# Performance work log

Measured on AMD Instinct MI355X. Metric: run time of the kernel, lower is better.

The kernel has to match this reference:

```python
import jax, jax.numpy as jnp
import numpy as np

B, N, H, W = 2, 1024, 128, 128
SH_K = 27  # (sh_degree+1)^2 * 3 for sh_degree=2
L_L1, L_SSIM, L_DEPTH, L_OPAC = 0.8, 0.2, 0.5, 0.01
C0 = 0.28209479177387814


def _quat_to_rot(q):
    # q: [..., 4] (w,x,y,z) -> [..., 3, 3]
    w, x, y, z = q[..., 0], q[..., 1], q[..., 2], q[..., 3]
    R = jnp.stack([1 - 2 * (y * y + z * z), 2 * (x * y - w * z), 2 * (x * z + w * y),
                   2 * (x * y + w * z), 1 - 2 * (x * x + z * z), 2 * (y * z - w * x),
                   2 * (x * z - w * y), 2 * (y * z + w * x), 1 - 2 * (x * x + y * y)], axis=-1)
    return R.reshape(q.shape[:-1] + (3, 3))


def _ssim_window(size=7, sigma=1.5):
    coords = np.arange(size, dtype=np.float32) - size // 2
    g = np.exp(-coords ** 2 / (2 * sigma ** 2))
    g = g / g.sum()
    w2 = np.outer(g, g).astype(np.float32)
    return jnp.asarray(np.broadcast_to(w2[None, None], (3, 1, size, size)))  # OIHW, groups=3


def _dwconv(img, w):
    return jax.lax.conv_general_dilated(img, w, (1, 1), 'SAME',
                                        dimension_numbers=('NCHW', 'OIHW', 'NCHW'),
                                        feature_group_count=3)


def _ssim(img1, img2):
    C1, C2 = 0.01 ** 2, 0.03 ** 2
    w = _ssim_window()
    mu1, mu2 = _dwconv(img1, w), _dwconv(img2, w)
    s1 = _dwconv(img1 * img1, w) - mu1 ** 2
    s2 = _dwconv(img2 * img2, w) - mu2 ** 2
    s12 = _dwconv(img1 * img2, w) - mu1 * mu2
    return jnp.mean((2 * mu1 * mu2 + C1) * (2 * s12 + C2) /
                    ((mu1 ** 2 + mu2 ** 2 + C1) * (s1 + s2 + C2)))


def _render(gaussians, intrinsics):
    means = gaussians[:, :, :3]
    scales = gaussians[:, :, 3:6]
    rots = gaussians[:, :, 6:10]
    opac = gaussians[:, :, 10]        # [B,N]
    sh = gaussians[:, :, 11:]
    fx = intrinsics[:, 0, 0][:, None]
    fy = intrinsics[:, 1, 1][:, None]
    cx = intrinsics[:, 0, 2][:, None]
    cy = intrinsics[:, 1, 2][:, None]
    z = jnp.maximum(means[:, :, 2], 1e-4)
    px = fx * means[:, :, 0] / z + cx
    py = fy * means[:, :, 1] / z + cy
    # ---- 2D covariance (EWA) ----
    R = _quat_to_rot(rots)                               # [B,N,3,3]
    RS = R * scales[:, :, None, :]                        # R @ diag(s)
    cov3d = RS @ jnp.swapaxes(RS, -1, -2)
    zc = jnp.maximum(means[:, :, 2], 1e-6)
    zsq = zc * zc
    J = jnp.zeros(means.shape[:2] + (2, 3), means.dtype)
    J = J.at[:, :, 0, 0].set(fx / zc)
    J = J.at[:, :, 0, 2].set(-fx * means[:, :, 0] / zsq)
    J = J.at[:, :, 1, 1].set(fy / zc)
    J = J.at[:, :, 1, 2].set(-fy * means[:, :, 1] / zsq)
    cov2d = J @ cov3d @ jnp.swapaxes(J, -1, -2) + 0.3 * jnp.eye(2, dtype=means.dtype)
    det = jnp.maximum(cov2d[:, :, 0, 0] * cov2d[:, :, 1, 1] -
                      cov2d[:, :, 0, 1] * cov2d[:, :, 1, 0], 1e-8)
    inv00 = cov2d[:, :, 1, 1] / det
    inv11 = cov2d[:, :, 0, 0] / det
    inv01 = -cov2d[:, :, 0, 1] / det
    colors = jnp.clip(sh[:, :, :3] * C0 + 0.5, 0.0, 1.0)  # [B,N,3]
    # ---- dense per-pixel splatting ----
    gy = jnp.arange(H, dtype=means.dtype)
    gx = jnp.arange(W, dtype=means.dtype)
    dx = gx[None, None, None, :] - px[:, :, None, None]   # [B,N,1,W] -> bcast [B,N,H,W]
    dy = gy[None, None, :, None] - py[:, :, None, None]
    power = -0.5 * (inv00[:, :, None, None] * dx * dx +
                    2.0 * inv01[:, :, None, None] * dx * dy +
                    inv11[:, :, None, None] * dy * dy)
    alpha = jnp.exp(jnp.clip(power, -10.0, 0.0)) * opac[:, :, None, None]
    alpha = jnp.minimum(alpha, 0.99)
    # ---- depth sort + front-to-back compositing ----
    order = jnp.argsort(z, axis=1)
    alpha_s = jnp.take_along_axis(alpha, order[:, :, None, None], axis=1)
    colors_s = jnp.take_along_axis(colors, order[:, :, None], axis=1)
    depth_s = jnp.take_along_axis(z, order, axis=1)
    cp = jnp.cumprod(1.0 - alpha_s, axis=1)
    Tr = jnp.concatenate([jnp.ones_like(alpha_s[:, :1]), cp[:, :-1]], axis=1)
    weights = Tr * alpha_s                               # [B,N,H,W]
    rgb = jnp.clip(jnp.einsum('bnhw,bnc->bchw', weights, colors_s), 0.0, 1.0)
    depth = jnp.sum(weights * depth_s[:, :, None, None], axis=1, keepdims=True)
    return rgb, depth


def setup_inputs() -> dict:
    key = jax.random.key(0)
    k = jax.random.split(key, 8)
    xy = jax.random.normal(k[0], (B, N, 2)) * 1.0
    zc = jax.random.uniform(k[1], (B, N, 1), minval=0.5, maxval=4.0)
    scales = jax.random.uniform(k[2], (B, N, 3), minval=0.01, maxval=0.1)
    q = jax.random.normal(k[3], (B, N, 4))
    q = q / jnp.linalg.norm(q, axis=-1, keepdims=True)
    opac = jax.nn.sigmoid(jax.random.normal(k[4], (B, N, 1)))
    sh = jax.random.normal(k[5], (B, N, SH_K)) * 0.3
    gaussians = jnp.concatenate([xy, zc, scales, q, opac, sh], axis=-1)  # [B,N,38]
    intr = jnp.tile(jnp.array([[120.0, 0.0, 64.0], [0.0, 120.0, 64.0], [0.0, 0.0, 1.0]],
                              dtype=jnp.float32)[None], (B, 1, 1))
    target_rgb = jax.random.uniform(k[6], (B, 3, H, W))
    target_depth = jax.random.uniform(k[7], (B, 1, H, W), minval=0.5, maxval=4.0)
    return {'gaussians': gaussians, 'intrinsics': intr,
            'target_rgb': target_rgb, 'target_depth': target_depth}


def reference(gaussians, intrinsics, target_rgb, target_depth):
    rgb, depth = _render(gaussians, intrinsics)
    l1_rgb = jnp.mean(jnp.abs(rgb - target_rgb))
    ssim_val = _ssim(rgb, target_rgb)
    l1_depth = jnp.mean(jnp.abs(depth - target_depth))
    o = jnp.clip(gaussians[:, :, 10:11], 1e-6, 1.0 - 1e-6)
    opacity_reg = jnp.mean(-(o * jnp.log(o) + (1.0 - o) * jnp.log(1.0 - o)))
    loss = (L_L1 * l1_rgb + L_SSIM * (1.0 - ssim_val) +
            L_DEPTH * l1_depth + L_OPAC * opacity_reg)
    return loss
```

## Files before the change

### kernel.cpp

```cpp
#include <hip/hip_runtime.h>

#define NB 2
#define NG 1024
#define HEIGHT 128
#define WIDTH 128
#define HW (HEIGHT * WIDTH)
#define E10 4.5399931e-05f

#define REC_S 0
#define P_ENT 32768
#define P_L1D 32800
#define P_SSS 33312
#define P_SSL 33696
#define CNT_I 34080
#define RGBOF 34084

__device__ inline float blk_reduce(float v, float* sh) {
    for (int off = 32; off > 0; off >>= 1) v += __shfl_down(v, off, 64);
    int lane = threadIdx.x & 63;
    int w = threadIdx.x >> 6;
    __syncthreads();
    if (lane == 0) sh[w] = v;
    __syncthreads();
    float s = 0.f;
    if (threadIdx.x == 0) {
        int nw = (blockDim.x + 63) >> 6;
        for (int i = 0; i < nw; i++) s += sh[i];
    }
    return s;
}

__global__ __launch_bounds__(256) void k_prerank(const float* __restrict__ g,
                                                 const float* __restrict__ intr,
                                                 float* __restrict__ ws) {
    __shared__ __align__(16) unsigned long long zkey[NG];
    __shared__ int sp[256];
    int bid = blockIdx.x;
    int b = bid >> 4;
    int grp = bid & 15;
    int tid = threadIdx.x;

#pragma unroll
    for (int q = 0; q < 4; q++) {
        int j = tid + q * 256;
        float z = fmaxf(g[(size_t)((b << 10) + j) * 38 + 2], 1e-4f);
        zkey[j] = ((unsigned long long)__float_as_uint(z) << 10) | (unsigned)j;
    }
    __syncthreads();

    int il = (grp << 6) + (tid & 63);
    int jq = tid >> 6;
    unsigned long long ki = zkey[il];
    int rank = 0;
    int j0 = jq << 8;
#pragma unroll 4
    for (int j = j0; j < j0 + 256; j += 2) {
        ulonglong2 kk = *(const ulonglong2*)(zkey + j);
        rank += (kk.x < ki);
        rank += (kk.y < ki);
    }
    sp[tid] = rank;
    __syncthreads();

    if (tid < 64) {
        int r = sp[tid] + sp[tid + 64] + sp[tid + 128] + sp[tid + 192];
        int idx = (b << 10) + il;
        const float* row = g + (size_t)idx * 38;
        float mx = row[0], my = row[1], mz = row[2];
        float sx = row[3], sy = row[4], sz = row[5];
        float qw = row[6], qx = row[7], qy = row[8], qz = row[9];
        float op = row[10];
        float sh0 = row[11], sh1 = row[12], sh2 = row[13];
        float fx = intr[b * 9 + 0], fy = intr[b * 9 + 4];
        float cx = intr[b * 9 + 2], cy = intr[b * 9 + 5];

        float z = fmaxf(mz, 1e-4f);
        float px = fx * mx / z + cx;
        float py = fy * my / z + cy;

        float r00 = 1.f - 2.f * (qy * qy + qz * qz), r01 = 2.f * (qx * qy - qw * qz), r02 = 2.f * (qx * qz + qw * qy);
        float r10 = 2.f * (qx * qy + qw * qz), r11 = 1.f - 2.f * (qx * qx + qz * qz), r12 = 2.f * (qy * qz - qw * qx);
        float r20 = 2.f * (qx * qz - qw * qy), r21 = 2.f * (qy * qz + qw * qx), r22 = 1.f - 2.f * (qx * qx + qy * qy);
        float a00 = r00 * sx, a01 = r01 * sy, a02 = r02 * sz;
        float a10 = r10 * sx, a11 = r11 * sy, a12 = r12 * sz;
        float a20 = r20 * sx, a21 = r21 * sy, a22 = r22 * sz;
        float m00 = a00 * a00 + a01 * a01 + a02 * a02;
        float m01 = a00 * a10 + a01 * a11 + a02 * a12;
        float m02 = a00 * a20 + a01 * a21 + a02 * a22;
        float m11 = a10 * a10 + a11 * a11 + a12 * a12;
        float m12 = a10 * a20 + a11 * a21 + a12 * a22;
        float m22 = a20 * a20 + a21 * a21 + a22 * a22;

        float zc = fmaxf(mz, 1e-6f);
        float aJ = fx / zc, bJ = -fx * mx / (zc * zc);
        float cJ = fy / zc, dJ = -fy * my / (zc * zc);
        float c00 = aJ * aJ * m00 + 2.f * aJ * bJ * m02 + bJ * bJ * m22 + 0.3f;
        float c01 = cJ * (aJ * m01 + bJ * m12) + dJ * (aJ * m02 + bJ * m22);
        float c11 = cJ * cJ * m11 + 2.f * cJ * dJ * m12 + dJ * dJ * m22 + 0.3f;
        float det = fmaxf(c00 * c11 - c01 * c01, 1e-8f);
        float i00 = c11 / det;
        float i11 = c00 / det;
        float i01 = -c01 / det;

        const float C0c = 0.28209479177387814f;
        float col0 = fminf(fmaxf(sh0 * C0c + 0.5f, 0.f), 1.f);
        float col1 = fminf(fmaxf(sh1 * C0c + 0.5f, 0.f), 1.f);
        float col2 = fminf(fmaxf(sh2 * C0c + 0.5f, 0.f), 1.f);

        float hx = sqrtf(20.f * c00);
        float hy = sqrtf(20.f * c11);

        float* rec = ws + REC_S + (size_t)((b << 10) + r) * 16;
        ((float4*)rec)[0] = make_float4(px, py, hx, hy);
        ((float4*)rec)[1] = make_float4(i00, i01, i11, op);
        ((float4*)rec)[2] = make_float4(col0, col1, col2, z);

        float o = fminf(fmaxf(op, 1e-6f), 1.f - 1e-6f);
        float ent = -(o * logf(o) + (1.f - o) * logf(1.f - o));
        for (int off = 32; off > 0; off >>= 1) ent += __shfl_down(ent, off, 64);
        if (tid == 0) ws[P_ENT + bid] = ent;
    }
    if (bid == 0 && tid == 0) ((int*)ws)[CNT_I] = 0;
}

__global__ __launch_bounds__(1024, 8) void k_render(const float* __restrict__ tgt_d,
                                                    float* __restrict__ ws) {
    __shared__ float4 sPa[NG + 1];
    __shared__ float sPud[NG + 1];
    __shared__ unsigned short slist[NG];
    __shared__ int swcnt[16];
    __shared__ float sagg[16 * 5];
    __shared__ float comb[5][1024];

    int tid = threadIdx.x;
    int lane = tid & 63;
    int wv = tid >> 6;
    int blk = blockIdx.x;
    int b = blk >> 8;
    int tt = blk & 255;
    int x0 = (tt & 15) * 8, y0 = (tt >> 4) * 8;
    int x = x0 + (lane & 7), y = y0 + (lane >> 3);
    float xf = (float)x, yf = (float)y;
    float x0f = (float)x0, x1f = x0f + 7.f;
    float y0f = (float)y0, y1f = y0f + 7.f;

    const float* recs = ws + REC_S + (size_t)(b << 10) * 16;

    const float* rec = recs + (size_t)tid * 16;
    float4 q0 = ((const float4*)rec)[0];
    float4 q1 = ((const float4*)rec)[1];
    float4 q2 = ((const float4*)rec)[2];

    bool ov = (q0.x + q0.z >= x0f) && (q0.x - q0.z <= x1f) &&
              (q0.y + q0.w >= y0f) && (q0.y - q0.w <= y1f);
    unsigned long long mask = __ballot(ov);
    int loff = __popcll(mask & ((1ull << lane) - 1ull));
    if (lane == 0) swcnt[wv] = (int)__popcll(mask);

    float a10 = E10 * q1.w;
    float t = 1.f - a10;
    float ur = a10 * q2.x, ug = a10 * q2.y, ub = a10 * q2.z, ud = a10 * q2.w;
#pragma unroll
    for (int off = 1; off < 64; off <<= 1) {
        float pt = __shfl_up(t, off, 64);
        float pr = __shfl_up(ur, off, 64);
        float pg = __shfl_up(ug, off, 64);
        float pb = __shfl_up(ub, off, 64);
        float pd = __shfl_up(ud, off, 64);
        if (lane >= off) {
            ur = pr + pt * ur; ug = pg + pt * ug;
            ub = pb + pt * ub; ud = pd + pt * ud;
            t = pt * t;
        }
    }
    if (lane == 63) {
        sagg[wv * 5 + 0] = t;  sagg[wv * 5 + 1] = ur; sagg[wv * 5 + 2] = ug;
        sagg[wv * 5 + 3] = ub; sagg[wv * 5 + 4] = ud;
    }
    __syncthreads();

    int woff = 0, cnt = 0;
#pragma unroll
    for (int i = 0; i < 16; i++) {
        int ci = swcnt[i];
        woff += (i < wv) ? ci : 0;
        cnt += ci;
    }
    if (ov) slist[woff + loff] = (unsigned short)tid;

    float Pt = 1.f, Pur = 0.f, Pug = 0.f, Pub = 0.f, Pud0 = 0.f;
    for (int i = 0; i < wv; i++) {
        float at = sagg[i * 5], ar = sagg[i * 5 + 1], ag = sagg[i * 5 + 2];
        float ab = sagg[i * 5 + 3], ad = sagg[i * 5 + 4];
        Pur = Pur + Pt * ar; Pug = Pug + Pt * ag;
        Pub = Pub + Pt * ab; Pud0 = Pud0 + Pt * ad;
        Pt = Pt * at;
    }
    sPa[tid + 1] = make_float4(Pt * t, Pur + Pt * ur, Pug + Pt * ug, Pub + Pt * ub);
    sPud[tid + 1] = Pud0 + Pt * ud;
    if (tid == 0) {
        sPa[0] = make_float4(1.f, 0.f, 0.f, 0.f);
        sPud[0] = 0.f;
    }
    __syncthreads();

    int m = (cnt + 15) >> 4;
    int p0 = wv * m; if (p0 > cnt) p0 = cnt;
    int p1 = p0 + m; if (p1 > cnt) p1 = cnt;
    int s0 = (p0 == 0) ? 0 : (int)slist[p0 - 1] + 1;

    float4 Pa = sPa[s0];
    float Pud = sPud[s0];
    float inv0 = 1.f / Pa.x;
    float Pur2 = Pa.y, Pug2 = Pa.z, Pub2 = Pa.w;

    float tau = 1.f, cr = 0.f, cgn = 0.f, cb = 0.f, cd = 0.f;
    for (int p = p0; p < p1; p++) {
        int r = (int)slist[p];
        float4 Qa = sPa[r];
        float Qud = sPud[r];
        const float* rp = recs + (size_t)r * 16;
        float4 g0 = ((const float4*)rp)[0];
        float4 g1 = ((const float4*)rp)[1];
        float4 g2 = ((const float4*)rp)[2];
        float kap = tau * inv0;
        cr += kap * (Qa.y - Pur2);
        cgn += kap * (Qa.z - Pug2);
        cb += kap * (Qa.w - Pub2);
        cd += kap * (Qud - Pud);
        float dx = xf - g0.x, dy = yf - g0.y;
        float q = g1.x * dx * dx + 2.f * g1.y * dx * dy + g1.z * dy * dy;
        float pw = fminf(fmaxf(-0.5f * q, -10.f), 0.f);
        float a = fminf(__expf(pw) * g1.w, 0.99f);
        float w = kap * Qa.x * a;
        cr += w * g2.x; cgn += w * g2.y; cb += w * g2.z; cd += w * g2.w;
        float a10i = E10 * g1.w;
        tau *= (1.f - a) * (1.f + a10i * (1.f + a10i));
        float s = Qa.x * a10i;
        Pur2 = Qa.y + s * g2.x;
        Pug2 = Qa.z + s * g2.y;
        Pub2 = Qa.w + s * g2.z;
        Pud = Qud + s * g2.w;
    }
    int e0 = (wv == 15) ? NG : ((p1 == 0) ? 0 : (int)slist[p1 - 1] + 1);
    float4 Ea = sPa[e0];
    float Eud = sPud[e0];
    float kapf = tau * inv0;
    cr += kapf * (Ea.y - Pur2);
    cgn += kapf * (Ea.z - Pug2);
    cb += kapf * (Ea.w - Pub2);
    cd += kapf * (Eud - Pud);
    float T = tau * Ea.x * inv0;

    comb[0][tid] = T;
    comb[1][tid] = cr;
    comb[2][tid] = cgn;
    comb[3][tid] = cb;
    comb[4][tid] = cd;
    __syncthreads();

    if (tid < 64) {
        float T0 = comb[0][tid], r0 = comb[1][tid], g0 = comb[2][tid];
        float b0 = comb[3][tid], d0 = comb[4][tid];
#pragma unroll
        for (int sgi = 1; sgi < 16; sgi++) {
            int j = sgi * 64 + tid;
            r0 += T0 * comb[1][j];
            g0 += T0 * comb[2][j];
            b0 += T0 * comb[3][j];
            d0 += T0 * comb[4][j];
            T0 *= comb[0][j];
        }
        r0 = fminf(fmaxf(r0, 0.f), 1.f);
        g0 = fminf(fmaxf(g0, 0.f), 1.f);
        b0 = fminf(fmaxf(b0, 0.f), 1.f);
        float* rgb = ws + RGBOF;
        rgb[((b * 3 + 0) * HEIGHT + y) * WIDTH + x] = r0;
        rgb[((b * 3 + 1) * HEIGHT + y) * WIDTH + x] = g0;
        rgb[((b * 3 + 2) * HEIGHT + y) * WIDTH + x] = b0;
        float l1d = fabsf(d0 - tgt_d[(b * HEIGHT + y) * WIDTH + x]);
        for (int off = 32; off > 0; off >>= 1) l1d += __shfl_down(l1d, off, 64);
        if (tid == 0) ws[P_L1D + blk] = l1d;
    }
}

__global__ __launch_bounds__(256) void k_ssim_final(const float* __restrict__ tgt_rgb,
                                                    float* __restrict__ ws,
                                                    float* __restrict__ out) {
    __shared__ float sh[8];
    __shared__ int sflag;
    int bid = blockIdx.x;
    int idx = bid * 256 + threadIdx.x;
    const float* img1 = ws + RGBOF;
    int bc = idx >> 14;
    int pix = idx & (HW - 1);
    int y = pix >> 7, x = pix & 127;

    float gg[7];
    float gs = 0.f;
#pragma unroll
    for (int i = 0; i < 7; i++) {
        float c = (float)(i - 3);
        gg[i] = __expf(-c * c / 4.5f);
        gs += gg[i];
    }
#pragma unroll
    for (int i = 0; i < 7; i++) gg[i] /= gs;

    float mu1 = 0.f, mu2 = 0.f, s11 = 0.f, s22 = 0.f, s12 = 0.f;
    int plane = bc * HW;
#pragma unroll
    for (int dy = -3; dy <= 3; dy++) {
        int yy = y + dy;
#pragma unroll
        for (int dx = -3; dx <= 3; dx++) {
            int xx = x + dx;
            float w = gg[dy + 3] * gg[dx + 3];
            float i1 = 0.f, i2 = 0.f;
            if (yy >= 0 && yy < HEIGHT && xx >= 0 && xx < WIDTH) {
                int o = plane + yy * WIDTH + xx;
                i1 = img1[o];
                i2 = tgt_rgb[o];
            }
            mu1 += w * i1;
            mu2 += w * i2;
            s11 += w * i1 * i1;
            s22 += w * i2 * i2;
            s12 += w * i1 * i2;
        }
    }
    float v1 = s11 - mu1 * mu1;
    float v2 = s22 - mu2 * mu2;
    float cv = s12 - mu1 * mu2;
    const float C1 = 1e-4f, C2 = 9e-4f;
    float ssim = ((2.f * mu1 * mu2 + C1) * (2.f * cv + C2)) /
                 ((mu1 * mu1 + mu2 * mu2 + C1) * (v1 + v2 + C2));
    float l1 = fabsf(img1[idx] - tgt_rgb[idx]);

    float s_ssim = blk_reduce(ssim, sh);
    float s_l1 = blk_reduce(l1, sh);

    if (threadIdx.x == 0) {
        ws[P_SSS + bid] = s_ssim;
        ws[P_SSL + bid] = s_l1;
        __threadfence();
        int old = atomicAdd((int*)ws + CNT_I, 1);
        sflag = (old == 383) ? 1 : 0;
    }
    __syncthreads();
    if (sflag) {
        __threadfence();
        float d = 0.f, ss = 0.f, sl = 0.f, e = 0.f;
        for (int i = threadIdx.x; i < 512; i += 256) d += ws[P_L1D + i];
        for (int i = threadIdx.x; i < 384; i += 256) { ss += ws[P_SSS + i]; sl += ws[P_SSL + i]; }
        if (threadIdx.x < 32) e = ws[P_ENT + threadIdx.x];
        float rd_ = blk_reduce(d, sh);
        float rss = blk_reduce(ss, sh);
        float rsl = blk_reduce(sl, sh);
        float re = blk_reduce(e, sh);
        if (threadIdx.x == 0) {
            float l1r = rsl / (float)(NB * 3 * HW);
            float ssimv = rss / (float)(NB * 3 * HW);
            float l1d = rd_ / (float)(NB * HW);
            float opa = re / (float)(NB * NG);
            out[0] = 0.8f * l1r + 0.2f * (1.f - ssimv) + 0.5f * l1d + 0.01f * opa;
        }
    }
}

extern "C" void kernel_launch(void* const* d_in, const int* in_sizes, int n_in,
                              void* d_out, int out_size, void* d_ws, size_t ws_size,
                              hipStream_t stream) {
    const float* g = (const float*)d_in[0];
    const float* intr = (const float*)d_in[1];
    const float* trgb = (const float*)d_in[2];
    const float* tdep = (const float*)d_in[3];
    float* ws = (float*)d_ws;
    float* out = (float*)d_out;

    hipLaunchKernelGGL(k_prerank, dim3(32), dim3(256), 0, stream, g, intr, ws);
    hipLaunchKernelGGL(k_render, dim3(NB * 256), dim3(1024), 0, stream, tdep, ws);
    hipLaunchKernelGGL(k_ssim_final, dim3((NB * 3 * HW) / 256), dim3(256), 0, stream, trgb, ws, out);
}
```

Before: 95.94 us.

## Tile SSIM in shared memory with padded image, shuffle-scan wave prefixes, prefetch list index

```diff
diff --git a/kernel.cpp b/kernel.cpp
--- a/kernel.cpp
+++ b/kernel.cpp
@@ -6,14 +6,16 @@
 #define WIDTH 128
 #define HW (HEIGHT * WIDTH)
 #define E10 4.5399931e-05f
+#define PW 134
+#define PPLANE (PW * PW)
 
 #define REC_S 0
 #define P_ENT 32768
 #define P_L1D 32800
 #define P_SSS 33312
-#define P_SSL 33696
-#define CNT_I 34080
-#define RGBOF 34084
+#define P_SSL 33504
+#define CNT_I 33696
+#define RGBOF 33700
 
 __device__ inline float blk_reduce(float v, float* sh) {
     for (int off = 32; off > 0; off >>= 1) v += __shfl_down(v, off, 64);
@@ -120,6 +122,8 @@
         for (int off = 32; off > 0; off >>= 1) ent += __shfl_down(ent, off, 64);
         if (tid == 0) ws[P_ENT + bid] = ent;
     }
+    for (int i = bid * 256 + tid; i < 6 * PPLANE; i += 32 * 256)
+        ws[RGBOF + i] = 0.f;
     if (bid == 0 && tid == 0) ((int*)ws)[CNT_I] = 0;
 }
 
@@ -188,16 +192,39 @@
     }
     if (ov) slist[woff + loff] = (unsigned short)tid;
 
-    float Pt = 1.f, Pur = 0.f, Pug = 0.f, Pub = 0.f, Pud0 = 0.f;
-    for (int i = 0; i < wv; i++) {
-        float at = sagg[i * 5], ar = sagg[i * 5 + 1], ag = sagg[i * 5 + 2];
-        float ab = sagg[i * 5 + 3], ad = sagg[i * 5 + 4];
-        Pur = Pur + Pt * ar; Pug = Pug + Pt * ag;
-        Pub = Pub + Pt * ab; Pud0 = Pud0 + Pt * ad;
-        Pt = Pt * at;
-    }
-    sPa[tid + 1] = make_float4(Pt * t, Pur + Pt * ur, Pug + Pt * ug, Pub + Pt * ub);
-    sPud[tid + 1] = Pud0 + Pt * ud;
+    if (tid < 16) {
+        float at = sagg[tid * 5 + 0], ar = sagg[tid * 5 + 1], ag = sagg[tid * 5 + 2];
+        float ab = sagg[tid * 5 + 3], ad = sagg[tid * 5 + 4];
+#pragma unroll
+        for (int off = 1; off < 16; off <<= 1) {
+            float pt = __shfl_up(at, off, 16);
+            float pr = __shfl_up(ar, off, 16);
+            float pg = __shfl_up(ag, off, 16);
+            float pb = __shfl_up(ab, off, 16);
+            float pd = __shfl_up(ad, off, 16);
+            if (tid >= off) {
+                ar = pr + pt * ar; ag = pg + pt * ag;
+                ab = pb + pt * ab; ad = pd + pt * ad;
+                at = pt * at;
+            }
+        }
+        float eat = __shfl_up(at, 1, 16);
+        float ear = __shfl_up(ar, 1, 16);
+        float eag = __shfl_up(ag, 1, 16);
+        float eab = __shfl_up(ab, 1, 16);
+        float ead = __shfl_up(ad, 1, 16);
+        if (tid == 0) { eat = 1.f; ear = 0.f; eag = 0.f; eab = 0.f; ead = 0.f; }
+        sagg[tid * 5 + 0] = eat; sagg[tid * 5 + 1] = ear; sagg[tid * 5 + 2] = eag;
+        sagg[tid * 5 + 3] = eab; sagg[tid * 5 + 4] = ead;
+    }
+    __syncthreads();
+
+    {
+        float Pt = sagg[wv * 5 + 0], Pur = sagg[wv * 5 + 1], Pug = sagg[wv * 5 + 2];
+        float Pub = sagg[wv * 5 + 3], Pud0 = sagg[wv * 5 + 4];
+        sPa[tid + 1] = make_float4(Pt * t, Pur + Pt * ur, Pug + Pt * ug, Pub + Pt * ub);
+        sPud[tid + 1] = Pud0 + Pt * ud;
+    }
     if (tid == 0) {
         sPa[0] = make_float4(1.f, 0.f, 0.f, 0.f);
         sPud[0] = 0.f;
@@ -215,8 +242,9 @@
     float Pur2 = Pa.y, Pug2 = Pa.z, Pub2 = Pa.w;
 
     float tau = 1.f, cr = 0.f, cgn = 0.f, cb = 0.f, cd = 0.f;
+    int r = (p0 < p1) ? (int)slist[p0] : 0;
     for (int p = p0; p < p1; p++) {
-        int r = (int)slist[p];
+        int rn = (p + 1 < p1) ? (int)slist[p + 1] : 0;
         float4 Qa = sPa[r];
         float Qud = sPud[r];
         const float* rp = recs + (size_t)r * 16;
@@ -241,6 +269,7 @@
         Pug2 = Qa.z + s * g2.y;
         Pub2 = Qa.w + s * g2.z;
         Pud = Qud + s * g2.w;
+        r = rn;
     }
     int e0 = (wv == 15) ? NG : ((p1 == 0) ? 0 : (int)slist[p1 - 1] + 1);
     float4 Ea = sPa[e0];
@@ -275,9 +304,10 @@
         g0 = fminf(fmaxf(g0, 0.f), 1.f);
         b0 = fminf(fmaxf(b0, 0.f), 1.f);
         float* rgb = ws + RGBOF;
-        rgb[((b * 3 + 0) * HEIGHT + y) * WIDTH + x] = r0;
-        rgb[((b * 3 + 1) * HEIGHT + y) * WIDTH + x] = g0;
-        rgb[((b * 3 + 2) * HEIGHT + y) * WIDTH + x] = b0;
+        int pofs = (y + 3) * PW + (x + 3);
+        rgb[(b * 3 + 0) * PPLANE + pofs] = r0;
+        rgb[(b * 3 + 1) * PPLANE + pofs] = g0;
+        rgb[(b * 3 + 2) * PPLANE + pofs] = b0;
         float l1d = fabsf(d0 - tgt_d[(b * HEIGHT + y) * WIDTH + x]);
         for (int off = 32; off > 0; off >>= 1) l1d += __shfl_down(l1d, off, 64);
         if (tid == 0) ws[P_L1D + blk] = l1d;
@@ -287,14 +317,29 @@
 __global__ __launch_bounds__(256) void k_ssim_final(const float* __restrict__ tgt_rgb,
                                                     float* __restrict__ ws,
                                                     float* __restrict__ out) {
+    __shared__ float s1[14 * 70];
+    __shared__ float s2[14 * 70];
     __shared__ float sh[8];
     __shared__ int sflag;
     int bid = blockIdx.x;
-    int idx = bid * 256 + threadIdx.x;
-    const float* img1 = ws + RGBOF;
-    int bc = idx >> 14;
-    int pix = idx & (HW - 1);
-    int y = pix >> 7, x = pix & 127;
+    int tid = threadIdx.x;
+    int p = bid >> 5;
+    int sy = (bid >> 1) & 15;
+    int hx2 = bid & 1;
+    int y0 = sy * 8, x0 = hx2 * 64;
+
+    const float* img1p = ws + RGBOF + (size_t)p * PPLANE;
+    const float* tgtp = tgt_rgb + (size_t)p * HW;
+    for (int i = tid; i < 14 * 70; i += 256) {
+        int r = i / 70, c = i - r * 70;
+        s1[i] = img1p[(y0 + r) * PW + (x0 + c)];
+        int yy = y0 + r - 3, xx = x0 + c - 3;
+        float v = 0.f;
+        if (yy >= 0 && yy < HEIGHT && xx >= 0 && xx < WIDTH)
+            v = tgtp[yy * WIDTH + xx];
+        s2[i] = v;
+    }
+    __syncthreads();
 
     float gg[7];
     float gs = 0.f;
@@ -307,58 +352,60 @@
 #pragma unroll
     for (int i = 0; i < 7; i++) gg[i] /= gs;
 
-    float mu1 = 0.f, mu2 = 0.f, s11 = 0.f, s22 = 0.f, s12 = 0.f;
-    int plane = bc * HW;
-#pragma unroll
-    for (int dy = -3; dy <= 3; dy++) {
-        int yy = y + dy;
-#pragma unroll
-        for (int dx = -3; dx <= 3; dx++) {
-            int xx = x + dx;
-            float w = gg[dy + 3] * gg[dx + 3];
-            float i1 = 0.f, i2 = 0.f;
-            if (yy >= 0 && yy < HEIGHT && xx >= 0 && xx < WIDTH) {
-                int o = plane + yy * WIDTH + xx;
-                i1 = img1[o];
-                i2 = tgt_rgb[o];
+    int row = tid >> 5;
+    int colb = (tid & 31) * 2;
+    float ssim_acc = 0.f, l1_acc = 0.f;
+#pragma unroll
+    for (int j = 0; j < 2; j++) {
+        int c = colb + j;
+        float mu1 = 0.f, mu2 = 0.f, s11 = 0.f, s22 = 0.f, s12 = 0.f;
+#pragma unroll
+        for (int dy = 0; dy < 7; dy++) {
+            int rb = (row + dy) * 70 + c;
+#pragma unroll
+            for (int dx = 0; dx < 7; dx++) {
+                float w = gg[dy] * gg[dx];
+                float i1 = s1[rb + dx];
+                float i2 = s2[rb + dx];
+                mu1 += w * i1;
+                mu2 += w * i2;
+                s11 += w * i1 * i1;
+                s22 += w * i2 * i2;
+                s12 += w * i1 * i2;
             }
-            mu1 += w * i1;
-            mu2 += w * i2;
-            s11 += w * i1 * i1;
-            s22 += w * i2 * i2;
-            s12 += w * i1 * i2;
         }
-    }
-    float v1 = s11 - mu1 * mu1;
-    float v2 = s22 - mu2 * mu2;
-    float cv = s12 - mu1 * mu2;
-    const float C1 = 1e-4f, C2 = 9e-4f;
-    float ssim = ((2.f * mu1 * mu2 + C1) * (2.f * cv + C2)) /
-                 ((mu1 * mu1 + mu2 * mu2 + C1) * (v1 + v2 + C2));
-    float l1 = fabsf(img1[idx] - tgt_rgb[idx]);
-
-    float s_ssim = blk_reduce(ssim, sh);
-    float s_l1 = blk_reduce(l1, sh);
-
-    if (threadIdx.x == 0) {
+        float v1 = s11 - mu1 * mu1;
+        float v2 = s22 - mu2 * mu2;
+        float cv = s12 - mu1 * mu2;
+        const float C1 = 1e-4f, C2 = 9e-4f;
+        ssim_acc += ((2.f * mu1 * mu2 + C1) * (2.f * cv + C2)) /
+                    ((mu1 * mu1 + mu2 * mu2 + C1) * (v1 + v2 + C2));
+        int ctr = (row + 3) * 70 + c + 3;
+        l1_acc += fabsf(s1[ctr] - s2[ctr]);
+    }
+
+    float s_ssim = blk_reduce(ssim_acc, sh);
+    float s_l1 = blk_reduce(l1_acc, sh);
+
+    if (tid == 0) {
         ws[P_SSS + bid] = s_ssim;
         ws[P_SSL + bid] = s_l1;
         __threadfence();
         int old = atomicAdd((int*)ws + CNT_I, 1);
-        sflag = (old == 383) ? 1 : 0;
+        sflag = (old == 191) ? 1 : 0;
     }
     __syncthreads();
     if (sflag) {
         __threadfence();
         float d = 0.f, ss = 0.f, sl = 0.f, e = 0.f;
-        for (int i = threadIdx.x; i < 512; i += 256) d += ws[P_L1D + i];
-        for (int i = threadIdx.x; i < 384; i += 256) { ss += ws[P_SSS + i]; sl += ws[P_SSL + i]; }
-        if (threadIdx.x < 32) e = ws[P_ENT + threadIdx.x];
+        for (int i = tid; i < 512; i += 256) d += ws[P_L1D + i];
+        if (tid < 192) { ss = ws[P_SSS + tid]; sl = ws[P_SSL + tid]; }
+        if (tid < 32) e = ws[P_ENT + tid];
         float rd_ = blk_reduce(d, sh);
         float rss = blk_reduce(ss, sh);
         float rsl = blk_reduce(sl, sh);
         float re = blk_reduce(e, sh);
-        if (threadIdx.x == 0) {
+        if (tid == 0) {
             float l1r = rsl / (float)(NB * 3 * HW);
             float ssimv = rss / (float)(NB * 3 * HW);
             float l1d = rd_ / (float)(NB * HW);
@@ -380,5 +427,5 @@
 
     hipLaunchKernelGGL(k_prerank, dim3(32), dim3(256), 0, stream, g, intr, ws);
     hipLaunchKernelGGL(k_render, dim3(NB * 256), dim3(1024), 0, stream, tdep, ws);
-    hipLaunchKernelGGL(k_ssim_final, dim3((NB * 3 * HW) / 256), dim3(256), 0, stream, trgb, ws, out);
+    hipLaunchKernelGGL(k_ssim_final, dim3(192), dim3(256), 0, stream, trgb, ws, out);
 }
```

Result: faster. 92.82 us (-3.2%).
